# Kernel tuning notes

Hardware: AMD Instinct MI355X
Metric: run time of the kernel (lower is better)

The kernel has to match this reference:

```python
import jax, jax.numpy as jnp
import numpy as np

EPS = 1e-6
HEADS = 16


def _layernorm(x, weight=None):
    mu = jnp.mean(x, axis=-1, keepdims=True)
    var = jnp.var(x, axis=-1, keepdims=True)
    y = (x - mu) / jnp.sqrt(var + EPS)
    return y if weight is None else y * weight


def _apply_rope(x, position):
    # x: [b, h, t, e]; position: [t, e//4, 2] (cos, sin pairs)
    e = x.shape[-1]
    t = x.shape[-2]
    x_rope, x_pass = x[..., : e // 2], x[..., e // 2 :]
    xr = x_rope.reshape(*x_rope.shape[:-1], -1, 2)  # [b,h,t,e//4,2]
    pos = position[:t].reshape(1, 1, t, -1, 2)
    cos, sin = pos[..., 0], pos[..., 1]
    x0, x1 = xr[..., 0], xr[..., 1]
    rot = jnp.stack([x0 * cos - x1 * sin, x1 * cos + x0 * sin], axis=-1)
    rot = rot.reshape(*rot.shape[:-2], -1)
    return jnp.concatenate([rot.astype(x.dtype), x_pass], axis=-1)


def setup_inputs() -> dict:
    key = jax.random.key(0)
    ks = jax.random.split(key, 8)
    B, T, D, TD = 8, 1024, 1024, 1024
    e = D // HEADS
    s = 0.02
    return {
        "x": jax.random.normal(ks[0], (B, T, D), jnp.float32),
        "time": jax.random.normal(ks[1], (B, 1, TD), jnp.float32),
        "position": jax.random.normal(ks[2], (T, e // 4, 2), jnp.float32),
        "mod_w": jax.random.normal(ks[3], (TD, 3 * D), jnp.float32) * s,
        "mod_b": jax.random.normal(ks[4], (3 * D,), jnp.float32) * s,
        "w_qkv": jax.random.normal(ks[5], (D, 3 * D), jnp.float32) * s,
        "w_out": jax.random.normal(ks[6], (D, D), jnp.float32) * s,
        "q_norm_w": jnp.ones((e,), jnp.float32),
        "k_norm_w": jnp.ones((e,), jnp.float32),
    }


def reference(x, time, position, mod_w, mod_b, w_qkv, w_out, q_norm_w, k_norm_w):
    B, T, D = x.shape
    H = HEADS
    e = D // H
    # AdaLN modulation
    h = _layernorm(x)
    mod = jax.nn.silu(time) @ mod_w + mod_b  # [B,1,3D]
    shift, scale, gate = jnp.split(mod, 3, axis=-1)
    h = h * (scale + 1.0) + shift
    # QKV projection; rearrange 'b t (n h e) -> n b h t e'
    qkv = (h @ w_qkv).reshape(B, T, 3, H, e).transpose(2, 0, 3, 1, 4)
    q, k, v = qkv[0], qkv[1], qkv[2]
    q = _apply_rope(_layernorm(q, q_norm_w), position)
    k = _apply_rope(_layernorm(k, k_norm_w), position)
    # SDPA
    scores = jnp.einsum("bhqe,bhke->bhqk", q, k) / jnp.sqrt(jnp.asarray(e, q.dtype))
    attn = jax.nn.softmax(scores, axis=-1)
    o = jnp.einsum("bhqk,bhke->bhqe", attn, v)
    o = o.transpose(0, 2, 1, 3).reshape(B, T, D)  # 'b h t e -> b t (h e)'
    return (o @ w_out) * gate
```

## Files before the change

kernel.cpp:

```cpp
#include <hip/hip_runtime.h>

typedef short bf16x8 __attribute__((ext_vector_type(8)));
typedef float f32x4 __attribute__((ext_vector_type(4)));

#define LN_EPS 1e-6f
#define QSCALE 0.1803368801111143f

static __device__ __forceinline__ float bf2f(unsigned short u) {
    union { unsigned int i; float f; } v; v.i = ((unsigned int)u) << 16; return v.f;
}
static __device__ __forceinline__ unsigned short f2bf(float f) {
    union { float ff; unsigned int i; } v; v.ff = f;
    return (unsigned short)((v.i + 0x7FFFu + ((v.i >> 16) & 1u)) >> 16);
}
static __device__ __forceinline__ void gl_lds16(const unsigned short* g, unsigned short* l) {
    __builtin_amdgcn_global_load_lds((__attribute__((address_space(1))) void*)g,
                                     (__attribute__((address_space(3))) void*)l,
                                     16, 0, 0);
}

__global__ __launch_bounds__(256) void prep_kernel(const float* __restrict__ w_qkv,
                                                   unsigned short* __restrict__ wqkvT,
                                                   const float* __restrict__ w_out,
                                                   unsigned short* __restrict__ woutT,
                                                   const float* __restrict__ timep,
                                                   const float* __restrict__ mod_w,
                                                   const float* __restrict__ mod_b,
                                                   float* __restrict__ mod) {
    __shared__ __align__(16) char sm[5248];
    const int bid = blockIdx.x;
    if (bid < 4096) {
        const float* src; unsigned short* dst; int C, c0, r0;
        if (bid < 3072) { src = w_qkv; dst = wqkvT; C = 3072; c0 = (bid % 96) * 32; r0 = (bid / 96) * 32; }
        else { int i2 = bid - 3072; src = w_out; dst = woutT; C = 1024; c0 = (i2 & 31) * 32; r0 = (i2 >> 5) * 32; }
        unsigned short (*t)[33] = (unsigned short(*)[33])sm;
        int tx = threadIdx.x & 31, ty = threadIdx.x >> 5;
        #pragma unroll
        for (int i = 0; i < 4; ++i) {
            int r = ty + i * 8;
            t[r][tx] = f2bf(src[(size_t)(r0 + r) * C + c0 + tx]);
        }
        __syncthreads();
        #pragma unroll
        for (int i = 0; i < 4; ++i) {
            int c = ty + i * 8;
            dst[(size_t)(c0 + c) * 1024 + r0 + tx] = t[tx][c];
        }
    } else {
        const int mb = bid - 4096;
        float* st = (float*)sm;
        float (*part)[33] = (float(*)[33])(sm + 4096);
        const int b = mb / 96;
        const int jb = mb % 96;
        const int tid = threadIdx.x;
        const int j = jb * 32 + (tid & 31);
        const int sub = tid >> 5;
        for (int i = tid; i < 1024; i += 256) {
            float t = timep[b * 1024 + i];
            st[i] = t / (1.0f + __expf(-t));
        }
        __syncthreads();
        float acc = 0.f;
        const int k0 = sub * 128;
        #pragma unroll 4
        for (int m = 0; m < 128; ++m)
            acc = fmaf(st[k0 + m], mod_w[(size_t)(k0 + m) * 3072 + j], acc);
        part[sub][tid & 31] = acc;
        __syncthreads();
        if (tid < 32) {
            float s = mod_b[jb * 32 + tid];
            #pragma unroll
            for (int p = 0; p < 8; ++p) s += part[p][tid];
            mod[b * 3072 + jb * 32 + tid] = s;
        }
    }
}

__global__ __launch_bounds__(256) void ln_mod_kernel(const float* __restrict__ x,
                                                     const float* __restrict__ mod,
                                                     unsigned short* __restrict__ h) {
    int row = blockIdx.x * 4 + (threadIdx.x >> 6);
    int lane = threadIdx.x & 63;
    int b = row >> 10;
    const float* xr = x + (size_t)row * 1024;
    float4 v[4];
    float s = 0.f, ss = 0.f;
    #pragma unroll
    for (int j = 0; j < 4; ++j) {
        v[j] = *reinterpret_cast<const float4*>(xr + j * 256 + lane * 4);
        s  += v[j].x + v[j].y + v[j].z + v[j].w;
        ss += v[j].x * v[j].x + v[j].y * v[j].y + v[j].z * v[j].z + v[j].w * v[j].w;
    }
    #pragma unroll
    for (int o = 32; o >= 1; o >>= 1) { s += __shfl_xor(s, o); ss += __shfl_xor(ss, o); }
    float mean = s * (1.0f / 1024.0f);
    float rstd = rsqrtf(ss * (1.0f / 1024.0f) - mean * mean + LN_EPS);
    const float* mb = mod + b * 3072;
    #pragma unroll
    for (int j = 0; j < 4; ++j) {
        int d = j * 256 + lane * 4;
        float4 shf = *reinterpret_cast<const float4*>(mb + d);
        float4 scl = *reinterpret_cast<const float4*>(mb + 1024 + d);
        ushort4 o4;
        o4.x = f2bf((v[j].x - mean) * rstd * (scl.x + 1.0f) + shf.x);
        o4.y = f2bf((v[j].y - mean) * rstd * (scl.y + 1.0f) + shf.y);
        o4.z = f2bf((v[j].z - mean) * rstd * (scl.z + 1.0f) + shf.z);
        o4.w = f2bf((v[j].w - mean) * rstd * (scl.w + 1.0f) + shf.w);
        *reinterpret_cast<ushort4*>(h + (size_t)row * 1024 + d) = o4;
    }
}

static __device__ __forceinline__ void gemm_mainloop(const unsigned short* __restrict__ A,
                                                     const unsigned short* __restrict__ Bt,
                                                     int m0, int n0,
                                                     unsigned short* As, unsigned short* Bs,
                                                     f32x4 (&acc)[4][4]) {
    const int tid = threadIdx.x;
    const int wid = tid >> 6, lane = tid & 63;
    const int wr = wid >> 1, wc = wid & 1;
    const int lr = lane & 15, lks = lane >> 4;
    const int gofs = (lane >> 3) * 1024 + (((lane & 7) ^ (lane >> 3)) * 8);
    const unsigned short* Ag = A  + (size_t)(m0 + wid * 32) * 1024 + gofs;
    const unsigned short* Bg = Bt + (size_t)(n0 + wid * 32) * 1024 + gofs;
    unsigned short* AsW = As + wid * 32 * 64;
    unsigned short* BsW = Bs + wid * 32 * 64;
    for (int k0 = 0; k0 < 1024; k0 += 64) {
        __syncthreads();
        #pragma unroll
        for (int j = 0; j < 4; ++j) {
            gl_lds16(Ag + k0 + j * 8192, AsW + j * 512);
            gl_lds16(Bg + k0 + j * 8192, BsW + j * 512);
        }
        __syncthreads();
        #pragma unroll
        for (int ks = 0; ks < 2; ++ks) {
            bf16x8 af[4], bfr[4];
            #pragma unroll
            for (int mi = 0; mi < 4; ++mi) {
                int row = wr * 64 + mi * 16 + lr;
                int ss = (ks * 4 + lks) ^ (row & 7);
                af[mi] = *reinterpret_cast<const bf16x8*>(As + row * 64 + ss * 8);
            }
            #pragma unroll
            for (int ni = 0; ni < 4; ++ni) {
                int row = wc * 64 + ni * 16 + lr;
                int ss = (ks * 4 + lks) ^ (row & 7);
                bfr[ni] = *reinterpret_cast<const bf16x8*>(Bs + row * 64 + ss * 8);
            }
            #pragma unroll
            for (int mi = 0; mi < 4; ++mi)
                #pragma unroll
                for (int ni = 0; ni < 4; ++ni)
                    acc[mi][ni] = __builtin_amdgcn_mfma_f32_16x16x32_bf16(af[mi], bfr[ni], acc[mi][ni], 0, 0, 0);
        }
    }
}

__global__ __launch_bounds__(256) void gemm_qkv_mfma(const unsigned short* __restrict__ A,
                                                     const unsigned short* __restrict__ Bt,
                                                     unsigned short* __restrict__ qb,
                                                     unsigned short* __restrict__ kb,
                                                     unsigned short* __restrict__ vb) {
    __shared__ __align__(16) unsigned short smem[16640];
    unsigned short* As = smem;
    unsigned short* Bs = smem + 8192;
    const int bid = blockIdx.y * 24 + blockIdx.x;
    const int xcd = bid & 7, idx = bid >> 3;
    const int m0 = (xcd * 8 + (idx & 7)) * 128;
    const int n0 = (idx >> 3) * 128;
    const int tid = threadIdx.x;
    const int wid = tid >> 6, lane = tid & 63;
    const int wr = wid >> 1, wc = wid & 1;
    const int lr = lane & 15, g = lane >> 4;
    const int which = n0 >> 10;
    f32x4 acc[4][4] = {};
    gemm_mainloop(A, Bt, m0, n0, As, Bs, acc);
    __syncthreads();
    #pragma unroll
    for (int mi = 0; mi < 4; ++mi)
    #pragma unroll
    for (int ni = 0; ni < 4; ++ni)
    #pragma unroll
    for (int r = 0; r < 4; ++r) {
        int row = wr * 64 + mi * 16 + g * 4 + r;
        int col = wc * 64 + ni * 16 + lr;
        if (which == 2) smem[col * 130 + row] = f2bf(acc[mi][ni][r]);
        else            smem[row * 130 + col] = f2bf(acc[mi][ni][r]);
    }
    __syncthreads();
    const int bb = m0 >> 10, tbase = m0 & 1023;
    if (which == 2) {
        #pragma unroll
        for (int p = 0; p < 8; ++p) {
            int seg = (tid >> 3) + p * 32;
            int erow = seg >> 1, half = seg & 1, sub = tid & 7;
            int4 v = *reinterpret_cast<const int4*>(smem + erow * 130 + half * 64 + sub * 8);
            int eg = (n0 & 1023) + erow;
            int hd = eg >> 6, ei = eg & 63;
            *reinterpret_cast<int4*>(vb + (((size_t)(bb * 16 + hd) * 64 + ei) << 10)
                                        + tbase + half * 64 + sub * 8) = v;
        }
    } else {
        unsigned short* dst = which == 0 ? qb : kb;
        #pragma unroll
        for (int p = 0; p < 8; ++p) {
            int seg = (tid >> 3) + p * 32;
            int row = seg >> 1, half = seg & 1, sub = tid & 7;
            int4 v = *reinterpret_cast<const int4*>(smem + row * 130 + half * 64 + sub * 8);
            int colb = n0 + half * 64;
            int hd = (colb & 1023) >> 6;
            int t = tbase + row;
            *reinterpret_cast<int4*>(dst + (((size_t)(bb * 16 + hd) * 1024 + t) << 6) + sub * 8) = v;
        }
    }
}

__global__ __launch_bounds__(256) void gemm_out_mfma(const unsigned short* __restrict__ A,
                                                     const unsigned short* __restrict__ Bt,
                                                     const float* __restrict__ mod,
                                                     float* __restrict__ out) {
    __shared__ __align__(16) unsigned short smem[16640];
    unsigned short* As = smem;
    unsigned short* Bs = smem + 8192;
    float* fsm = reinterpret_cast<float*>(smem);
    const int bid = blockIdx.y * 8 + blockIdx.x;
    const int xcd = bid & 7, idx = bid >> 3;
    const int m0 = (xcd * 8 + (idx & 7)) * 128;
    const int n0 = (idx >> 3) * 128;
    const int tid = threadIdx.x;
    const int wid = tid >> 6, lane = tid & 63;
    const int wr = wid >> 1, wc = wid & 1;
    const int lr = lane & 15, g = lane >> 4;
    f32x4 acc[4][4] = {};
    gemm_mainloop(A, Bt, m0, n0, As, Bs, acc);
    #pragma unroll
    for (int hp = 0; hp < 2; ++hp) {
        __syncthreads();
        if (wr == hp) {
            #pragma unroll
            for (int mi = 0; mi < 4; ++mi)
            #pragma unroll
            for (int ni = 0; ni < 4; ++ni)
            #pragma unroll
            for (int r = 0; r < 4; ++r)
                fsm[(mi * 16 + g * 4 + r) * 128 + wc * 64 + ni * 16 + lr] = acc[mi][ni][r];
        }
        __syncthreads();
        #pragma unroll
        for (int p = 0; p < 8; ++p) {
            int unit = tid + p * 256;
            int lrow = unit >> 5, sub = unit & 31;
            float4 v = *reinterpret_cast<const float4*>(fsm + lrow * 128 + sub * 4);
            int row = m0 + hp * 64 + lrow;
            int col = n0 + sub * 4;
            int bb = row >> 10;
            float4 gv = *reinterpret_cast<const float4*>(mod + bb * 3072 + 2048 + col);
            float4 o4;
            o4.x = v.x * gv.x; o4.y = v.y * gv.y; o4.z = v.z * gv.z; o4.w = v.w * gv.w;
            *reinterpret_cast<float4*>(out + (size_t)row * 1024 + col) = o4;
        }
    }
}

__global__ __launch_bounds__(256) void lnrope_kernel(unsigned short* __restrict__ qb,
                                                     unsigned short* __restrict__ kb,
                                                     const float* __restrict__ qw,
                                                     const float* __restrict__ kw,
                                                     const float* __restrict__ pos) {
    int gw = blockIdx.x * 4 + (threadIdx.x >> 6);
    int lane = threadIdx.x & 63;
    int half = gw >> 15;
    int rw = (gw * 4 + (lane >> 4)) & 131071;
    unsigned short* buf = half ? kb : qb;
    const float* w = half ? kw : qw;
    int t = rw & 1023;
    int c4 = (lane & 15) * 4;
    size_t idx = (size_t)rw * 64 + c4;
    ushort4 u = *reinterpret_cast<const ushort4*>(buf + idx);
    float f0 = bf2f(u.x), f1 = bf2f(u.y), f2 = bf2f(u.z), f3 = bf2f(u.w);
    float s1 = f0 + f1 + f2 + f3;
    float s2 = f0 * f0 + f1 * f1 + f2 * f2 + f3 * f3;
    #pragma unroll
    for (int o = 1; o <= 8; o <<= 1) { s1 += __shfl_xor(s1, o); s2 += __shfl_xor(s2, o); }
    float mean = s1 * (1.0f / 64.0f);
    float rstd = rsqrtf(s2 * (1.0f / 64.0f) - mean * mean + LN_EPS);
    float4 wv = *reinterpret_cast<const float4*>(w + c4);
    float y0 = (f0 - mean) * rstd * wv.x;
    float y1 = (f1 - mean) * rstd * wv.y;
    float y2 = (f2 - mean) * rstd * wv.z;
    float y3 = (f3 - mean) * rstd * wv.w;
    if (c4 < 32) {
        float4 p = *reinterpret_cast<const float4*>(pos + t * 32 + c4);
        float a;
        a = y0; y0 = a * p.x - y1 * p.y; y1 = y1 * p.x + a * p.y;
        a = y2; y2 = a * p.z - y3 * p.w; y3 = y3 * p.z + a * p.w;
    }
    const float SC = half ? 1.0f : QSCALE;
    ushort4 o;
    o.x = f2bf(y0 * SC); o.y = f2bf(y1 * SC); o.z = f2bf(y2 * SC); o.w = f2bf(y3 * SC);
    *reinterpret_cast<ushort4*>(buf + idx) = o;
}

__global__ __launch_bounds__(256) void attn_mfma_kernel(const unsigned short* __restrict__ qb,
                                                        const unsigned short* __restrict__ kb,
                                                        const unsigned short* __restrict__ vt,
                                                        unsigned short* __restrict__ ob) {
    __shared__ __align__(16) unsigned char smem[40960];
    unsigned short* KsB = (unsigned short*)smem;
    unsigned short* VsB = (unsigned short*)(smem + 16384);
    unsigned short* paQ = (unsigned short*)(smem + 32768);

    const int bid = blockIdx.x;
    const int swz = (bid & 7) * 256 + (bid >> 3);
    const int bh = swz >> 4;
    const int q0 = (swz & 15) * 64;
    const int b = bh >> 4, hd = bh & 15;
    const size_t base = (size_t)bh << 16;
    const int tid = threadIdx.x, wid = tid >> 6, lane = tid & 63;
    const int lr = lane & 15, g = lane >> 4;

    int kRd[2][4], pRd[2], pwOff[4][4];
    #pragma unroll
    for (int ks = 0; ks < 2; ++ks) {
        pRd[ks] = lr * 64 + (((ks * 4 + g) ^ (lr & 7)) * 8);
        #pragma unroll
        for (int nt = 0; nt < 4; ++nt)
            kRd[ks][nt] = (nt * 16 + lr) * 64 + (((ks * 4 + g) ^ (lr & 7)) * 8);
    }
    #pragma unroll
    for (int nt = 0; nt < 4; ++nt)
    #pragma unroll
    for (int r = 0; r < 4; ++r) {
        int q = g * 4 + r;
        pwOff[nt][r] = q * 64 + (((nt * 2 + (lr >> 3)) ^ (q & 7)) * 8) + (lr & 7);
    }

    const unsigned short* kSrc[2];
    const unsigned short* vSrc[2];
    #pragma unroll
    for (int p = 0; p < 2; ++p) {
        int idx = p * 256 + tid;
        int r = idx >> 3, sg = idx & 7;
        kSrc[p] = kb + base + (size_t)r * 64 + ((sg ^ (r & 7)) * 8);
        vSrc[p] = vt + base + (size_t)r * 1024 + ((sg ^ (r & 7)) * 8);
    }

    #pragma unroll
    for (int p = 0; p < 2; ++p) {
        gl_lds16(kSrc[p], KsB + p * 2048 + wid * 512);
        gl_lds16(vSrc[p], VsB + p * 2048 + wid * 512);
    }
    #pragma unroll
    for (int p = 0; p < 2; ++p) {
        int r = (tid >> 3) + p * 32;
        int sseg = tid & 7;
        int4 qv = *reinterpret_cast<const int4*>(qb + base + (size_t)(q0 + r) * 64 + sseg * 8);
        *reinterpret_cast<int4*>(paQ + r * 64 + ((sseg ^ (r & 7)) * 8)) = qv;
    }
    __syncthreads();
    bf16x8 af[2];
    #pragma unroll
    for (int ks = 0; ks < 2; ++ks) {
        int row = wid * 16 + lr;
        af[ks] = *reinterpret_cast<const bf16x8*>(paQ + row * 64 + (((ks * 4 + g) ^ (row & 7)) * 8));
    }
    __syncthreads();

    f32x4 acc[4] = {};
    float l_par[4] = {0.f, 0.f, 0.f, 0.f};
    unsigned short* pa_w = paQ + wid * 1024;
    const f32x4 zero4 = {0.f, 0.f, 0.f, 0.f};

    for (int cc = 0; cc < 16; ++cc) {
        const int cur = cc & 1;
        if (cc < 15) {
            const int kv1 = (cc + 1) * 64;
            unsigned short* Kd = KsB + (cur ^ 1) * 4096;
            unsigned short* Vd = VsB + (cur ^ 1) * 4096;
            #pragma unroll
            for (int p = 0; p < 2; ++p) {
                gl_lds16(kSrc[p] + (size_t)kv1 * 64, Kd + p * 2048 + wid * 512);
                gl_lds16(vSrc[p] + kv1,              Vd + p * 2048 + wid * 512);
            }
        }
        const unsigned short* Kc = KsB + cur * 4096;
        const unsigned short* Vc = VsB + cur * 4096;
        f32x4 s[4];
        __builtin_amdgcn_s_setprio(1);
        #pragma unroll
        for (int nt = 0; nt < 4; ++nt) {
            bf16x8 kf = *reinterpret_cast<const bf16x8*>(Kc + kRd[0][nt]);
            s[nt] = __builtin_amdgcn_mfma_f32_16x16x32_bf16(af[0], kf, zero4, 0, 0, 0);
        }
        #pragma unroll
        for (int nt = 0; nt < 4; ++nt) {
            bf16x8 kf = *reinterpret_cast<const bf16x8*>(Kc + kRd[1][nt]);
            s[nt] = __builtin_amdgcn_mfma_f32_16x16x32_bf16(af[1], kf, s[nt], 0, 0, 0);
        }
        __builtin_amdgcn_s_setprio(0);
        #pragma unroll
        for (int r = 0; r < 4; ++r)
        #pragma unroll
        for (int nt = 0; nt < 4; ++nt) {
            float e = exp2f(s[nt][r]);
            s[nt][r] = e;
            l_par[r] += e;
        }
        #pragma unroll
        for (int nt = 0; nt < 4; ++nt)
        #pragma unroll
        for (int r = 0; r < 4; ++r) {
            unsigned int pk;
            asm("v_cvt_pk_bf16_f32 %0, %1, %2" : "=v"(pk) : "v"(s[nt][r]), "v"(0.f));
            pa_w[pwOff[nt][r]] = (unsigned short)pk;
        }
        __builtin_amdgcn_s_setprio(1);
        #pragma unroll
        for (int ks = 0; ks < 2; ++ks) {
            bf16x8 paf = *reinterpret_cast<const bf16x8*>(pa_w + pRd[ks]);
            #pragma unroll
            for (int nt = 0; nt < 4; ++nt) {
                bf16x8 vf = *reinterpret_cast<const bf16x8*>(Vc + kRd[ks][nt]);
                acc[nt] = __builtin_amdgcn_mfma_f32_16x16x32_bf16(paf, vf, acc[nt], 0, 0, 0);
            }
        }
        __builtin_amdgcn_s_setprio(0);
        __syncthreads();
    }
    float inv[4];
    #pragma unroll
    for (int r = 0; r < 4; ++r) {
        float l = l_par[r];
        #pragma unroll
        for (int o = 1; o <= 8; o <<= 1) l += __shfl_xor(l, o);
        inv[r] = 1.0f / l;
    }
    #pragma unroll
    for (int nt = 0; nt < 4; ++nt)
    #pragma unroll
    for (int r = 0; r < 4; ++r) {
        int q = q0 + wid * 16 + g * 4 + r;
        int d = hd * 64 + nt * 16 + lr;
        ob[(size_t)(b * 1024 + q) * 1024 + d] = f2bf(acc[nt][r] * inv[r]);
    }
}

extern "C" void kernel_launch(void* const* d_in, const int* in_sizes, int n_in,
                              void* d_out, int out_size, void* d_ws, size_t ws_size,
                              hipStream_t stream) {
    const float* x      = (const float*)d_in[0];
    const float* timep  = (const float*)d_in[1];
    const float* pos    = (const float*)d_in[2];
    const float* mod_w  = (const float*)d_in[3];
    const float* mod_b  = (const float*)d_in[4];
    const float* w_qkv  = (const float*)d_in[5];
    const float* w_out  = (const float*)d_in[6];
    const float* qw     = (const float*)d_in[7];
    const float* kw     = (const float*)d_in[8];
    float* outp = (float*)d_out;

    char* ws = (char*)d_ws;
    float*          modbuf = (float*)ws;
    unsigned short* wqkvT  = (unsigned short*)(ws + 98304);
    unsigned short* woutT  = (unsigned short*)(ws + 6389760);
    unsigned short* hbuf   = (unsigned short*)(ws + 8486912);
    unsigned short* qbuf   = hbuf + 8388608;
    unsigned short* kbuf   = qbuf + 8388608;
    unsigned short* vbuf   = kbuf + 8388608;
    unsigned short* obuf   = hbuf;

    prep_kernel<<<4864, 256, 0, stream>>>(w_qkv, wqkvT, w_out, woutT, timep, mod_w, mod_b, modbuf);
    ln_mod_kernel<<<2048, 256, 0, stream>>>(x, modbuf, hbuf);
    gemm_qkv_mfma<<<dim3(24, 64), 256, 0, stream>>>(hbuf, wqkvT, qbuf, kbuf, vbuf);
    lnrope_kernel<<<16384, 256, 0, stream>>>(qbuf, kbuf, qw, kw, pos);
    attn_mfma_kernel<<<2048, 256, 0, stream>>>(qbuf, kbuf, vbuf, obuf);
    gemm_out_mfma<<<dim3(8, 64), 256, 0, stream>>>(obuf, woutT, modbuf, outp);
}
```

Baseline: 199.3 us.

## Process 128 query rows per attention block with 8 waves sharing K/V tiles

New measurement: 192.1 us. 1.04x faster.

```diff
diff --git a/kernel.cpp b/kernel.cpp
--- a/kernel.cpp
+++ b/kernel.cpp
@@ -301,19 +301,19 @@
     *reinterpret_cast<ushort4*>(buf + idx) = o;
 }
 
-__global__ __launch_bounds__(256) void attn_mfma_kernel(const unsigned short* __restrict__ qb,
+__global__ __launch_bounds__(512) void attn_mfma_kernel(const unsigned short* __restrict__ qb,
                                                         const unsigned short* __restrict__ kb,
                                                         const unsigned short* __restrict__ vt,
                                                         unsigned short* __restrict__ ob) {
-    __shared__ __align__(16) unsigned char smem[40960];
+    __shared__ __align__(16) unsigned char smem[49152];
     unsigned short* KsB = (unsigned short*)smem;
     unsigned short* VsB = (unsigned short*)(smem + 16384);
     unsigned short* paQ = (unsigned short*)(smem + 32768);
 
     const int bid = blockIdx.x;
-    const int swz = (bid & 7) * 256 + (bid >> 3);
-    const int bh = swz >> 4;
-    const int q0 = (swz & 15) * 64;
+    const int swz = (bid & 7) * 128 + (bid >> 3);
+    const int bh = swz >> 3;
+    const int q0 = (swz & 7) * 128;
     const int b = bh >> 4, hd = bh & 15;
     const size_t base = (size_t)bh << 16;
     const int tid = threadIdx.x, wid = tid >> 6, lane = tid & 63;
@@ -335,27 +335,17 @@
         pwOff[nt][r] = q * 64 + (((nt * 2 + (lr >> 3)) ^ (q & 7)) * 8) + (lr & 7);
     }
 
-    const unsigned short* kSrc[2];
-    const unsigned short* vSrc[2];
+    const int sr = tid >> 3, ssg = tid & 7;
+    const unsigned short* kSrc = kb + base + (size_t)sr * 64 + ((ssg ^ (sr & 7)) * 8);
+    const unsigned short* vSrc = vt + base + (size_t)sr * 1024 + ((ssg ^ (sr & 7)) * 8);
+
+    gl_lds16(kSrc, KsB + wid * 512);
+    gl_lds16(vSrc, VsB + wid * 512);
     #pragma unroll
     for (int p = 0; p < 2; ++p) {
-        int idx = p * 256 + tid;
-        int r = idx >> 3, sg = idx & 7;
-        kSrc[p] = kb + base + (size_t)r * 64 + ((sg ^ (r & 7)) * 8);
-        vSrc[p] = vt + base + (size_t)r * 1024 + ((sg ^ (r & 7)) * 8);
-    }
-
-    #pragma unroll
-    for (int p = 0; p < 2; ++p) {
-        gl_lds16(kSrc[p], KsB + p * 2048 + wid * 512);
-        gl_lds16(vSrc[p], VsB + p * 2048 + wid * 512);
-    }
-    #pragma unroll
-    for (int p = 0; p < 2; ++p) {
-        int r = (tid >> 3) + p * 32;
-        int sseg = tid & 7;
-        int4 qv = *reinterpret_cast<const int4*>(qb + base + (size_t)(q0 + r) * 64 + sseg * 8);
-        *reinterpret_cast<int4*>(paQ + r * 64 + ((sseg ^ (r & 7)) * 8)) = qv;
+        int r = (tid >> 3) + p * 64;
+        int4 qv = *reinterpret_cast<const int4*>(qb + base + (size_t)(q0 + r) * 64 + ssg * 8);
+        *reinterpret_cast<int4*>(paQ + r * 64 + ((ssg ^ (r & 7)) * 8)) = qv;
     }
     __syncthreads();
     bf16x8 af[2];
@@ -375,13 +365,8 @@
         const int cur = cc & 1;
         if (cc < 15) {
             const int kv1 = (cc + 1) * 64;
-            unsigned short* Kd = KsB + (cur ^ 1) * 4096;
-            unsigned short* Vd = VsB + (cur ^ 1) * 4096;
-            #pragma unroll
-            for (int p = 0; p < 2; ++p) {
-                gl_lds16(kSrc[p] + (size_t)kv1 * 64, Kd + p * 2048 + wid * 512);
-                gl_lds16(vSrc[p] + kv1,              Vd + p * 2048 + wid * 512);
-            }
+            gl_lds16(kSrc + (size_t)kv1 * 64, KsB + (cur ^ 1) * 4096 + wid * 512);
+            gl_lds16(vSrc + kv1,              VsB + (cur ^ 1) * 4096 + wid * 512);
         }
         const unsigned short* Kc = KsB + cur * 4096;
         const unsigned short* Vc = VsB + cur * 4096;
@@ -473,6 +458,6 @@
     ln_mod_kernel<<<2048, 256, 0, stream>>>(x, modbuf, hbuf);
     gemm_qkv_mfma<<<dim3(24, 64), 256, 0, stream>>>(hbuf, wqkvT, qbuf, kbuf, vbuf);
     lnrope_kernel<<<16384, 256, 0, stream>>>(qbuf, kbuf, qw, kw, pos);
-    attn_mfma_kernel<<<2048, 256, 0, stream>>>(qbuf, kbuf, vbuf, obuf);
+    attn_mfma_kernel<<<1024, 512, 0, stream>>>(qbuf, kbuf, vbuf, obuf);
     gemm_out_mfma<<<dim3(8, 64), 256, 0, stream>>>(obuf, woutT, modbuf, outp);
 }
```
